# Optimization experiments

Measured on AMD Instinct MI355X. Metric: run time of the kernel, lower is better.

Reference implementation:

```python
import jax, jax.numpy as jnp
import numpy as np

ALPHA = 0.2  # leaky-relu negative slope


def setup_inputs() -> dict:
    key = jax.random.key(0)
    k1, k2, k3, k4 = jax.random.split(key, 4)
    bs, L, D, Fin, Fout = 4, 20000, 16, 128, 128
    x = jax.random.normal(k1, (bs, L, Fin), dtype=jnp.float32)
    adj = jax.random.randint(k2, (bs, L, D), 0, L, dtype=jnp.int64)
    # xavier_normal-ish init for W [Fin, Fout] and a [2*Fout, 1]
    W = jax.random.normal(k3, (Fin, Fout), dtype=jnp.float32) * (1.414 * np.sqrt(2.0 / (Fin + Fout))).astype(np.float32)
    a = jax.random.normal(k4, (2 * Fout, 1), dtype=jnp.float32) * (1.414 * np.sqrt(2.0 / (2 * Fout + 1))).astype(np.float32)
    return {"x": x, "adj": adj, "W": W, "a": a}


def reference(x, adj, W, a):
    Fout = W.shape[1]
    # gather fixed-degree neighbor features: [bs, L, D, Fin]
    nbr = jax.vmap(lambda xb, ab: xb[ab])(x, adj)
    h = jnp.matmul(nbr, W)  # [bs, L, D, Fout]
    # a is applied to cat([h_neighbor, h_center]); split it instead of concatenating
    a1 = a[:Fout, 0]
    a2 = a[Fout:, 0]
    # h[:, :, 0, :] is the center node (first neighbor slot, repeat_interleave in torch)
    e = jnp.einsum('bldf,f->bld', h, a1) + jnp.einsum('blf,f->bl', h[:, :, 0, :], a2)[..., None]
    attn = jax.nn.softmax(jax.nn.leaky_relu(e, ALPHA), axis=-1)  # softmax over D
    out = jnp.einsum('bld,bldf->blf', attn, h)  # weighted aggregate [bs, L, Fout]
    return jax.nn.elu(out)  # concat=True branch
```

## Files before the change

### kernel.cpp

```cpp
#include <hip/hip_runtime.h>
#include <hip/hip_bf16.h>

#define LSEQ 20000
#define DEG  16
#define F    128
#define ALPHA 0.2f

typedef __bf16 bf16x8 __attribute__((ext_vector_type(8)));
typedef float  f32x4  __attribute__((ext_vector_type(4)));

__device__ __forceinline__ float bf_lo(unsigned int u) { return __uint_as_float(u << 16); }
__device__ __forceinline__ float bf_hi(unsigned int u) { return __uint_as_float(u & 0xffff0000u); }
__device__ __forceinline__ float elu_f(float v) { return v > 0.f ? v : __expf(v) - 1.f; }

__global__ __launch_bounds__(256) void gat_wt(const float* __restrict__ W,
                                              const float* __restrict__ a,
                                              __hip_bfloat16* __restrict__ wt,
                                              float* __restrict__ wa)
{
    const int t = blockIdx.x * 256 + threadIdx.x;
    for (int i = t; i < F * F; i += 16 * 256) {
        const int k = i >> 7, n = i & (F - 1);
        wt[n * F + k] = __float2bfloat16(W[i]);
    }
    if (blockIdx.x == 0 && threadIdx.x < F) {
        const int k = threadIdx.x;
        float acc1 = 0.f, acc2 = 0.f;
        for (int n = 0; n < F; ++n) {
            const float w = W[k * F + n];
            acc1 = fmaf(w, a[n],     acc1);
            acc2 = fmaf(w, a[F + n], acc2);
        }
        wa[k]     = acc1;
        wa[F + k] = acc2;
    }
}

__global__ __launch_bounds__(256, 5) void gat_gemm(const float* __restrict__ x,
                                                   const __hip_bfloat16* __restrict__ wt,
                                                   const float* __restrict__ wa,
                                                   __hip_bfloat16* __restrict__ y16,
                                                   float* __restrict__ s1,
                                                   float* __restrict__ s2)
{
    __shared__ __hip_bfloat16 wl[F][F];

    const int t    = threadIdx.x;
    const int lane = t & 63;
    const int wid  = t >> 6;
    const int i0   = (blockIdx.x * 4 + wid) * 16;
    const int m    = lane & 15;
    const int q    = lane >> 4;

    {
        const uint4* wg = reinterpret_cast<const uint4*>(wt);
        #pragma unroll
        for (int i = 0; i < 8; ++i) {
            const int g   = t + 256 * i;
            const int row = g >> 4;
            const int c8  = g & 15;
            *reinterpret_cast<uint4*>(&wl[row][((c8 ^ (row & 7)) * 8)]) = wg[g];
        }
    }

    const float* xr = x + (size_t)(i0 + m) * F + q * 8;
    float4 xf[8];
    #pragma unroll
    for (int kt = 0; kt < 4; ++kt) {
        xf[2*kt]   = *reinterpret_cast<const float4*>(xr + kt * 32);
        xf[2*kt+1] = *reinterpret_cast<const float4*>(xr + kt * 32 + 4);
    }

    float p1 = 0.f, p2 = 0.f;
    {
        const float* w1p = wa + q * 8;
        const float* w2p = wa + F + q * 8;
        #pragma unroll
        for (int kt = 0; kt < 4; ++kt) {
            const float4 u0 = *reinterpret_cast<const float4*>(w1p + kt * 32);
            const float4 u1 = *reinterpret_cast<const float4*>(w1p + kt * 32 + 4);
            const float4 v0 = *reinterpret_cast<const float4*>(w2p + kt * 32);
            const float4 v1 = *reinterpret_cast<const float4*>(w2p + kt * 32 + 4);
            const float4 xa = xf[2*kt], xb = xf[2*kt+1];
            p1 = fmaf(xa.x,u0.x,p1); p1 = fmaf(xa.y,u0.y,p1);
            p1 = fmaf(xa.z,u0.z,p1); p1 = fmaf(xa.w,u0.w,p1);
            p1 = fmaf(xb.x,u1.x,p1); p1 = fmaf(xb.y,u1.y,p1);
            p1 = fmaf(xb.z,u1.z,p1); p1 = fmaf(xb.w,u1.w,p1);
            p2 = fmaf(xa.x,v0.x,p2); p2 = fmaf(xa.y,v0.y,p2);
            p2 = fmaf(xa.z,v0.z,p2); p2 = fmaf(xa.w,v0.w,p2);
            p2 = fmaf(xb.x,v1.x,p2); p2 = fmaf(xb.y,v1.y,p2);
            p2 = fmaf(xb.z,v1.z,p2); p2 = fmaf(xb.w,v1.w,p2);
        }
    }
    p1 += __shfl_xor(p1, 16); p1 += __shfl_xor(p1, 32);
    p2 += __shfl_xor(p2, 16); p2 += __shfl_xor(p2, 32);
    if (lane < 16) {
        s1[i0 + m] = p1;
        s2[i0 + m] = p2;
    }

    bf16x8 bfr[4];
    #pragma unroll
    for (int kt = 0; kt < 4; ++kt) {
        const float4 qa = xf[2*kt], qb = xf[2*kt+1];
        bf16x8 f;
        f[0] = (__bf16)qa.x; f[1] = (__bf16)qa.y; f[2] = (__bf16)qa.z; f[3] = (__bf16)qa.w;
        f[4] = (__bf16)qb.x; f[5] = (__bf16)qb.y; f[6] = (__bf16)qb.z; f[7] = (__bf16)qb.w;
        bfr[kt] = f;
    }

    __syncthreads();

    #pragma unroll
    for (int ct = 0; ct < 8; ++ct) {
        union { uint4 u; bf16x8 v; } afr[4];
        const int row = ct * 16 + m;
        #pragma unroll
        for (int kt = 0; kt < 4; ++kt)
            afr[kt].u = *reinterpret_cast<const uint4*>(
                            &wl[row][(((kt * 4 + q) ^ (m & 7)) * 8)]);

        f32x4 acc = {0.f, 0.f, 0.f, 0.f};
        #pragma unroll
        for (int kt = 0; kt < 4; ++kt)
            acc = __builtin_amdgcn_mfma_f32_16x16x32_bf16(afr[kt].v, bfr[kt], acc, 0, 0, 0);

        union { uint2 u; __hip_bfloat162 h[2]; } pk;
        pk.h[0] = __float22bfloat162_rn(make_float2(acc[0], acc[1]));
        pk.h[1] = __float22bfloat162_rn(make_float2(acc[2], acc[3]));
        *reinterpret_cast<uint2*>(y16 + (size_t)(i0 + m) * F + ct * 16 + q * 4) = pk.u;
    }
}

__global__ __launch_bounds__(256, 4) void gat_attn(const int* __restrict__ adj,
                                                   const __hip_bfloat16* __restrict__ y16,
                                                   const float* __restrict__ s1,
                                                   const float* __restrict__ s2,
                                                   float* __restrict__ out)
{
    const int lane  = threadIdx.x & 63;
    const int wid   = threadIdx.x >> 6;
    const int x8    = blockIdx.x & 7;
    const int j     = blockIdx.x >> 3;
    const int batch = x8 >> 1;
    const int grp   = j * 2 + (x8 & 1);
    const int base  = batch * LSEQ;
    const int g0    = base + grp * 16 + wid * 4;
    const int d     = lane & 15;
    const int g16   = lane & 48;

    const int av = adj[(size_t)g0 * DEG + lane];

    const float sv = s1[base + av];
    float s2l = (d == 0) ? s2[base + av] : 0.f;
    const float s2v = __shfl(s2l, g16);
    const float e = sv + s2v;
    const float t = e > 0.f ? e : ALPHA * e;

    float mx = t;
    #pragma unroll
    for (int off = 1; off < 16; off <<= 1) mx = fmaxf(mx, __shfl_xor(mx, off));
    const float w = __expf(t - mx);
    float p = w;
    #pragma unroll
    for (int off = 1; off < 16; off <<= 1) p += __shfl_xor(p, off);
    const float attn = w / p;

    const char* yb = reinterpret_cast<const char*>(y16 + ((size_t)base << 7)) + d * 16;
    float acc[8] = {0.f, 0.f, 0.f, 0.f, 0.f, 0.f, 0.f, 0.f};

    uint4 va[8], vb[8];
    #pragma unroll
    for (int k = 0; k < 8; ++k) {
        const int r = __shfl(av, g16 + k);
        va[k] = *reinterpret_cast<const uint4*>(yb + ((size_t)r << 8));
    }
    #pragma unroll
    for (int k = 0; k < 8; ++k) {
        const int r = __shfl(av, g16 + 8 + k);
        vb[k] = *reinterpret_cast<const uint4*>(yb + ((size_t)r << 8));
    }

    #pragma unroll
    for (int k = 0; k < 8; ++k) {
        const float wk = __shfl(attn, g16 + k);
        const uint4 v = va[k];
        acc[0] = fmaf(wk, bf_lo(v.x), acc[0]);
        acc[1] = fmaf(wk, bf_hi(v.x), acc[1]);
        acc[2] = fmaf(wk, bf_lo(v.y), acc[2]);
        acc[3] = fmaf(wk, bf_hi(v.y), acc[3]);
        acc[4] = fmaf(wk, bf_lo(v.z), acc[4]);
        acc[5] = fmaf(wk, bf_hi(v.z), acc[5]);
        acc[6] = fmaf(wk, bf_lo(v.w), acc[6]);
        acc[7] = fmaf(wk, bf_hi(v.w), acc[7]);
    }
    #pragma unroll
    for (int k = 0; k < 8; ++k) {
        const float wk = __shfl(attn, g16 + 8 + k);
        const uint4 v = vb[k];
        acc[0] = fmaf(wk, bf_lo(v.x), acc[0]);
        acc[1] = fmaf(wk, bf_hi(v.x), acc[1]);
        acc[2] = fmaf(wk, bf_lo(v.y), acc[2]);
        acc[3] = fmaf(wk, bf_hi(v.y), acc[3]);
        acc[4] = fmaf(wk, bf_lo(v.z), acc[4]);
        acc[5] = fmaf(wk, bf_hi(v.z), acc[5]);
        acc[6] = fmaf(wk, bf_lo(v.w), acc[6]);
        acc[7] = fmaf(wk, bf_hi(v.w), acc[7]);
    }

    float* op = out + (size_t)(g0 + (lane >> 4)) * F + d * 8;
    const float4 o0 = make_float4(elu_f(acc[0]), elu_f(acc[1]),
                                  elu_f(acc[2]), elu_f(acc[3]));
    const float4 o1 = make_float4(elu_f(acc[4]), elu_f(acc[5]),
                                  elu_f(acc[6]), elu_f(acc[7]));
    *reinterpret_cast<float4*>(op)     = o0;
    *reinterpret_cast<float4*>(op + 4) = o1;
}

extern "C" void kernel_launch(void* const* d_in, const int* in_sizes, int n_in,
                              void* d_out, int out_size, void* d_ws, size_t ws_size,
                              hipStream_t stream) {
    const float* x   = (const float*)d_in[0];
    const int*   adj = (const int*)d_in[1];
    const float* W   = (const float*)d_in[2];
    const float* a   = (const float*)d_in[3];
    float* out = (float*)d_out;

    const int BL = in_sizes[0] / F;

    __hip_bfloat16* y16 = (__hip_bfloat16*)d_ws;
    float* s1 = (float*)((char*)d_ws + (size_t)BL * F * sizeof(__hip_bfloat16));
    float* s2 = s1 + BL;
    __hip_bfloat16* wt = (__hip_bfloat16*)(s2 + BL);
    float* wa = (float*)(wt + F * F);

    gat_wt  <<<16, 256, 0, stream>>>(W, a, wt, wa);
    gat_gemm<<<BL / 64, 256, 0, stream>>>(x, wt, wa, y16, s1, s2);
    gat_attn<<<BL / 16, 256, 0, stream>>>(adj, y16, s1, s2, out);
}
```

Baseline: 137.6 us.

## Fuse GEMM and attention kernels into persistent kernel with grid barrier

```diff
diff --git a/kernel.cpp b/kernel.cpp
--- a/kernel.cpp
+++ b/kernel.cpp
@@ -5,6 +5,7 @@
 #define DEG  16
 #define F    128
 #define ALPHA 0.2f
+#define GRID 1024
 
 typedef __bf16 bf16x8 __attribute__((ext_vector_type(8)));
 typedef float  f32x4  __attribute__((ext_vector_type(4)));
@@ -13,10 +14,11 @@
 __device__ __forceinline__ float bf_hi(unsigned int u) { return __uint_as_float(u & 0xffff0000u); }
 __device__ __forceinline__ float elu_f(float v) { return v > 0.f ? v : __expf(v) - 1.f; }
 
-__global__ __launch_bounds__(256) void gat_wt(const float* __restrict__ W,
-                                              const float* __restrict__ a,
-                                              __hip_bfloat16* __restrict__ wt,
-                                              float* __restrict__ wa)
+__global__ __launch_bounds__(256) void gat_prep(const float* __restrict__ W,
+                                                const float* __restrict__ a,
+                                                __hip_bfloat16* __restrict__ wt,
+                                                float* __restrict__ wa,
+                                                unsigned int* __restrict__ bar)
 {
     const int t = blockIdx.x * 256 + threadIdx.x;
     for (int i = t; i < F * F; i += 16 * 256) {
@@ -34,23 +36,27 @@
         wa[k]     = acc1;
         wa[F + k] = acc2;
     }
+    if (blockIdx.x == 15 && threadIdx.x == 0) *bar = 0u;
 }
 
-__global__ __launch_bounds__(256, 5) void gat_gemm(const float* __restrict__ x,
-                                                   const __hip_bfloat16* __restrict__ wt,
-                                                   const float* __restrict__ wa,
-                                                   __hip_bfloat16* __restrict__ y16,
-                                                   float* __restrict__ s1,
-                                                   float* __restrict__ s2)
+__global__ __launch_bounds__(256, 4) void gat_fused(
+    const float* __restrict__ x,
+    const int*   __restrict__ adj,
+    const __hip_bfloat16* __restrict__ wt,
+    const float* __restrict__ wa,
+    __hip_bfloat16* __restrict__ y16,
+    float* __restrict__ s1,
+    float* __restrict__ s2,
+    float* __restrict__ out,
+    unsigned int* __restrict__ bar,
+    int BL)
 {
     __shared__ __hip_bfloat16 wl[F][F];
 
+    const int bid  = blockIdx.x;
     const int t    = threadIdx.x;
     const int lane = t & 63;
     const int wid  = t >> 6;
-    const int i0   = (blockIdx.x * 4 + wid) * 16;
-    const int m    = lane & 15;
-    const int q    = lane >> 4;
 
     {
         const uint4* wg = reinterpret_cast<const uint4*>(wt);
@@ -62,159 +68,173 @@
             *reinterpret_cast<uint4*>(&wl[row][((c8 ^ (row & 7)) * 8)]) = wg[g];
         }
     }
-
-    const float* xr = x + (size_t)(i0 + m) * F + q * 8;
-    float4 xf[8];
-    #pragma unroll
-    for (int kt = 0; kt < 4; ++kt) {
-        xf[2*kt]   = *reinterpret_cast<const float4*>(xr + kt * 32);
-        xf[2*kt+1] = *reinterpret_cast<const float4*>(xr + kt * 32 + 4);
-    }
-
-    float p1 = 0.f, p2 = 0.f;
+    __syncthreads();
+
+    const int m = lane & 15;
+    const int q = lane >> 4;
+    const int NU = BL / 64;
+
+    for (int u = bid; u < NU; u += GRID) {
+        const int i0 = u * 64 + wid * 16;
+
+        const float* xr = x + (size_t)(i0 + m) * F + q * 8;
+        float4 xf[8];
+        #pragma unroll
+        for (int kt = 0; kt < 4; ++kt) {
+            xf[2*kt]   = *reinterpret_cast<const float4*>(xr + kt * 32);
+            xf[2*kt+1] = *reinterpret_cast<const float4*>(xr + kt * 32 + 4);
+        }
+
+        float p1 = 0.f, p2 = 0.f;
+        {
+            const float* w1p = wa + q * 8;
+            const float* w2p = wa + F + q * 8;
+            #pragma unroll
+            for (int kt = 0; kt < 4; ++kt) {
+                const float4 u0 = *reinterpret_cast<const float4*>(w1p + kt * 32);
+                const float4 u1 = *reinterpret_cast<const float4*>(w1p + kt * 32 + 4);
+                const float4 v0 = *reinterpret_cast<const float4*>(w2p + kt * 32);
+                const float4 v1 = *reinterpret_cast<const float4*>(w2p + kt * 32 + 4);
+                const float4 xa = xf[2*kt], xb = xf[2*kt+1];
+                p1 = fmaf(xa.x,u0.x,p1); p1 = fmaf(xa.y,u0.y,p1);
+                p1 = fmaf(xa.z,u0.z,p1); p1 = fmaf(xa.w,u0.w,p1);
+                p1 = fmaf(xb.x,u1.x,p1); p1 = fmaf(xb.y,u1.y,p1);
+                p1 = fmaf(xb.z,u1.z,p1); p1 = fmaf(xb.w,u1.w,p1);
+                p2 = fmaf(xa.x,v0.x,p2); p2 = fmaf(xa.y,v0.y,p2);
+                p2 = fmaf(xa.z,v0.z,p2); p2 = fmaf(xa.w,v0.w,p2);
+                p2 = fmaf(xb.x,v1.x,p2); p2 = fmaf(xb.y,v1.y,p2);
+                p2 = fmaf(xb.z,v1.z,p2); p2 = fmaf(xb.w,v1.w,p2);
+            }
+        }
+        p1 += __shfl_xor(p1, 16); p1 += __shfl_xor(p1, 32);
+        p2 += __shfl_xor(p2, 16); p2 += __shfl_xor(p2, 32);
+        if (lane < 16) {
+            s1[i0 + m] = p1;
+            s2[i0 + m] = p2;
+        }
+
+        bf16x8 bfr[4];
+        #pragma unroll
+        for (int kt = 0; kt < 4; ++kt) {
+            const float4 qa = xf[2*kt], qb = xf[2*kt+1];
+            bf16x8 f;
+            f[0] = (__bf16)qa.x; f[1] = (__bf16)qa.y; f[2] = (__bf16)qa.z; f[3] = (__bf16)qa.w;
+            f[4] = (__bf16)qb.x; f[5] = (__bf16)qb.y; f[6] = (__bf16)qb.z; f[7] = (__bf16)qb.w;
+            bfr[kt] = f;
+        }
+
+        #pragma unroll
+        for (int ct = 0; ct < 8; ++ct) {
+            union { uint4 u; bf16x8 v; } afr[4];
+            const int row = ct * 16 + m;
+            #pragma unroll
+            for (int kt = 0; kt < 4; ++kt)
+                afr[kt].u = *reinterpret_cast<const uint4*>(
+                                &wl[row][(((kt * 4 + q) ^ (m & 7)) * 8)]);
+
+            f32x4 acc = {0.f, 0.f, 0.f, 0.f};
+            #pragma unroll
+            for (int kt = 0; kt < 4; ++kt)
+                acc = __builtin_amdgcn_mfma_f32_16x16x32_bf16(afr[kt].v, bfr[kt], acc, 0, 0, 0);
+
+            union { uint2 u; __hip_bfloat162 h[2]; } pk;
+            pk.h[0] = __float22bfloat162_rn(make_float2(acc[0], acc[1]));
+            pk.h[1] = __float22bfloat162_rn(make_float2(acc[2], acc[3]));
+            *reinterpret_cast<uint2*>(y16 + (size_t)(i0 + m) * F + ct * 16 + q * 4) = pk.u;
+        }
+    }
+
+    __syncthreads();
+    if (t == 0) {
+        __threadfence();
+        atomicAdd(bar, 1u);
+        while (atomicAdd(bar, 0u) < (unsigned)GRID)
+            __builtin_amdgcn_s_sleep(2);
+        __threadfence();
+    }
+    __syncthreads();
+
     {
-        const float* w1p = wa + q * 8;
-        const float* w2p = wa + F + q * 8;
-        #pragma unroll
-        for (int kt = 0; kt < 4; ++kt) {
-            const float4 u0 = *reinterpret_cast<const float4*>(w1p + kt * 32);
-            const float4 u1 = *reinterpret_cast<const float4*>(w1p + kt * 32 + 4);
-            const float4 v0 = *reinterpret_cast<const float4*>(w2p + kt * 32);
-            const float4 v1 = *reinterpret_cast<const float4*>(w2p + kt * 32 + 4);
-            const float4 xa = xf[2*kt], xb = xf[2*kt+1];
-            p1 = fmaf(xa.x,u0.x,p1); p1 = fmaf(xa.y,u0.y,p1);
-            p1 = fmaf(xa.z,u0.z,p1); p1 = fmaf(xa.w,u0.w,p1);
-            p1 = fmaf(xb.x,u1.x,p1); p1 = fmaf(xb.y,u1.y,p1);
-            p1 = fmaf(xb.z,u1.z,p1); p1 = fmaf(xb.w,u1.w,p1);
-            p2 = fmaf(xa.x,v0.x,p2); p2 = fmaf(xa.y,v0.y,p2);
-            p2 = fmaf(xa.z,v0.z,p2); p2 = fmaf(xa.w,v0.w,p2);
-            p2 = fmaf(xb.x,v1.x,p2); p2 = fmaf(xb.y,v1.y,p2);
-            p2 = fmaf(xb.z,v1.z,p2); p2 = fmaf(xb.w,v1.w,p2);
-        }
-    }
-    p1 += __shfl_xor(p1, 16); p1 += __shfl_xor(p1, 32);
-    p2 += __shfl_xor(p2, 16); p2 += __shfl_xor(p2, 32);
-    if (lane < 16) {
-        s1[i0 + m] = p1;
-        s2[i0 + m] = p2;
-    }
-
-    bf16x8 bfr[4];
-    #pragma unroll
-    for (int kt = 0; kt < 4; ++kt) {
-        const float4 qa = xf[2*kt], qb = xf[2*kt+1];
-        bf16x8 f;
-        f[0] = (__bf16)qa.x; f[1] = (__bf16)qa.y; f[2] = (__bf16)qa.z; f[3] = (__bf16)qa.w;
-        f[4] = (__bf16)qb.x; f[5] = (__bf16)qb.y; f[6] = (__bf16)qb.z; f[7] = (__bf16)qb.w;
-        bfr[kt] = f;
-    }
-
-    __syncthreads();
-
-    #pragma unroll
-    for (int ct = 0; ct < 8; ++ct) {
-        union { uint4 u; bf16x8 v; } afr[4];
-        const int row = ct * 16 + m;
-        #pragma unroll
-        for (int kt = 0; kt < 4; ++kt)
-            afr[kt].u = *reinterpret_cast<const uint4*>(
-                            &wl[row][(((kt * 4 + q) ^ (m & 7)) * 8)]);
-
-        f32x4 acc = {0.f, 0.f, 0.f, 0.f};
-        #pragma unroll
-        for (int kt = 0; kt < 4; ++kt)
-            acc = __builtin_amdgcn_mfma_f32_16x16x32_bf16(afr[kt].v, bfr[kt], acc, 0, 0, 0);
-
-        union { uint2 u; __hip_bfloat162 h[2]; } pk;
-        pk.h[0] = __float22bfloat162_rn(make_float2(acc[0], acc[1]));
-        pk.h[1] = __float22bfloat162_rn(make_float2(acc[2], acc[3]));
-        *reinterpret_cast<uint2*>(y16 + (size_t)(i0 + m) * F + ct * 16 + q * 4) = pk.u;
-    }
-}
-
-__global__ __launch_bounds__(256, 4) void gat_attn(const int* __restrict__ adj,
-                                                   const __hip_bfloat16* __restrict__ y16,
-                                                   const float* __restrict__ s1,
-                                                   const float* __restrict__ s2,
-                                                   float* __restrict__ out)
-{
-    const int lane  = threadIdx.x & 63;
-    const int wid   = threadIdx.x >> 6;
-    const int x8    = blockIdx.x & 7;
-    const int j     = blockIdx.x >> 3;
-    const int batch = x8 >> 1;
-    const int grp   = j * 2 + (x8 & 1);
-    const int base  = batch * LSEQ;
-    const int g0    = base + grp * 16 + wid * 4;
-    const int d     = lane & 15;
-    const int g16   = lane & 48;
-
-    const int av = adj[(size_t)g0 * DEG + lane];
-
-    const float sv = s1[base + av];
-    float s2l = (d == 0) ? s2[base + av] : 0.f;
-    const float s2v = __shfl(s2l, g16);
-    const float e = sv + s2v;
-    const float t = e > 0.f ? e : ALPHA * e;
-
-    float mx = t;
-    #pragma unroll
-    for (int off = 1; off < 16; off <<= 1) mx = fmaxf(mx, __shfl_xor(mx, off));
-    const float w = __expf(t - mx);
-    float p = w;
-    #pragma unroll
-    for (int off = 1; off < 16; off <<= 1) p += __shfl_xor(p, off);
-    const float attn = w / p;
-
-    const char* yb = reinterpret_cast<const char*>(y16 + ((size_t)base << 7)) + d * 16;
-    float acc[8] = {0.f, 0.f, 0.f, 0.f, 0.f, 0.f, 0.f, 0.f};
-
-    uint4 va[8], vb[8];
-    #pragma unroll
-    for (int k = 0; k < 8; ++k) {
-        const int r = __shfl(av, g16 + k);
-        va[k] = *reinterpret_cast<const uint4*>(yb + ((size_t)r << 8));
-    }
-    #pragma unroll
-    for (int k = 0; k < 8; ++k) {
-        const int r = __shfl(av, g16 + 8 + k);
-        vb[k] = *reinterpret_cast<const uint4*>(yb + ((size_t)r << 8));
-    }
-
-    #pragma unroll
-    for (int k = 0; k < 8; ++k) {
-        const float wk = __shfl(attn, g16 + k);
-        const uint4 v = va[k];
-        acc[0] = fmaf(wk, bf_lo(v.x), acc[0]);
-        acc[1] = fmaf(wk, bf_hi(v.x), acc[1]);
-        acc[2] = fmaf(wk, bf_lo(v.y), acc[2]);
-        acc[3] = fmaf(wk, bf_hi(v.y), acc[3]);
-        acc[4] = fmaf(wk, bf_lo(v.z), acc[4]);
-        acc[5] = fmaf(wk, bf_hi(v.z), acc[5]);
-        acc[6] = fmaf(wk, bf_lo(v.w), acc[6]);
-        acc[7] = fmaf(wk, bf_hi(v.w), acc[7]);
-    }
-    #pragma unroll
-    for (int k = 0; k < 8; ++k) {
-        const float wk = __shfl(attn, g16 + 8 + k);
-        const uint4 v = vb[k];
-        acc[0] = fmaf(wk, bf_lo(v.x), acc[0]);
-        acc[1] = fmaf(wk, bf_hi(v.x), acc[1]);
-        acc[2] = fmaf(wk, bf_lo(v.y), acc[2]);
-        acc[3] = fmaf(wk, bf_hi(v.y), acc[3]);
-        acc[4] = fmaf(wk, bf_lo(v.z), acc[4]);
-        acc[5] = fmaf(wk, bf_hi(v.z), acc[5]);
-        acc[6] = fmaf(wk, bf_lo(v.w), acc[6]);
-        acc[7] = fmaf(wk, bf_hi(v.w), acc[7]);
-    }
-
-    float* op = out + (size_t)(g0 + (lane >> 4)) * F + d * 8;
-    const float4 o0 = make_float4(elu_f(acc[0]), elu_f(acc[1]),
-                                  elu_f(acc[2]), elu_f(acc[3]));
-    const float4 o1 = make_float4(elu_f(acc[4]), elu_f(acc[5]),
-                                  elu_f(acc[6]), elu_f(acc[7]));
-    *reinterpret_cast<float4*>(op)     = o0;
-    *reinterpret_cast<float4*>(op + 4) = o1;
+        const int d   = lane & 15;
+        const int g16 = lane & 48;
+        const int NV  = BL / 16;
+
+        for (int v = bid; v < NV; v += GRID) {
+            const int x8    = v & 7;
+            const int j     = v >> 3;
+            const int batch = x8 >> 1;
+            const int grp   = j * 2 + (x8 & 1);
+            const int base  = batch * LSEQ;
+            const int g0    = base + grp * 16 + wid * 4;
+
+            const int av = adj[(size_t)g0 * DEG + lane];
+
+            const float sv = s1[base + av];
+            float s2l = (d == 0) ? s2[base + av] : 0.f;
+            const float s2v = __shfl(s2l, g16);
+            const float e = sv + s2v;
+            const float tv = e > 0.f ? e : ALPHA * e;
+
+            float mx = tv;
+            #pragma unroll
+            for (int off = 1; off < 16; off <<= 1) mx = fmaxf(mx, __shfl_xor(mx, off));
+            const float w = __expf(tv - mx);
+            float p = w;
+            #pragma unroll
+            for (int off = 1; off < 16; off <<= 1) p += __shfl_xor(p, off);
+            const float attn = w / p;
+
+            const char* yb = reinterpret_cast<const char*>(y16 + ((size_t)base << 7)) + d * 16;
+            float acc[8] = {0.f, 0.f, 0.f, 0.f, 0.f, 0.f, 0.f, 0.f};
+
+            uint4 va[8], vb[8];
+            #pragma unroll
+            for (int k = 0; k < 8; ++k) {
+                const int r = __shfl(av, g16 + k);
+                va[k] = *reinterpret_cast<const uint4*>(yb + ((size_t)r << 8));
+            }
+            #pragma unroll
+            for (int k = 0; k < 8; ++k) {
+                const int r = __shfl(av, g16 + 8 + k);
+                vb[k] = *reinterpret_cast<const uint4*>(yb + ((size_t)r << 8));
+            }
+
+            #pragma unroll
+            for (int k = 0; k < 8; ++k) {
+                const float wk = __shfl(attn, g16 + k);
+                const uint4 vv = va[k];
+                acc[0] = fmaf(wk, bf_lo(vv.x), acc[0]);
+                acc[1] = fmaf(wk, bf_hi(vv.x), acc[1]);
+                acc[2] = fmaf(wk, bf_lo(vv.y), acc[2]);
+                acc[3] = fmaf(wk, bf_hi(vv.y), acc[3]);
+                acc[4] = fmaf(wk, bf_lo(vv.z), acc[4]);
+                acc[5] = fmaf(wk, bf_hi(vv.z), acc[5]);
+                acc[6] = fmaf(wk, bf_lo(vv.w), acc[6]);
+                acc[7] = fmaf(wk, bf_hi(vv.w), acc[7]);
+            }
+            #pragma unroll
+            for (int k = 0; k < 8; ++k) {
+                const float wk = __shfl(attn, g16 + 8 + k);
+                const uint4 vv = vb[k];
+                acc[0] = fmaf(wk, bf_lo(vv.x), acc[0]);
+                acc[1] = fmaf(wk, bf_hi(vv.x), acc[1]);
+                acc[2] = fmaf(wk, bf_lo(vv.y), acc[2]);
+                acc[3] = fmaf(wk, bf_hi(vv.y), acc[3]);
+                acc[4] = fmaf(wk, bf_lo(vv.z), acc[4]);
+                acc[5] = fmaf(wk, bf_hi(vv.z), acc[5]);
+                acc[6] = fmaf(wk, bf_lo(vv.w), acc[6]);
+                acc[7] = fmaf(wk, bf_hi(vv.w), acc[7]);
+            }
+
+            float* op = out + (size_t)(g0 + (lane >> 4)) * F + d * 8;
+            const float4 o0 = make_float4(elu_f(acc[0]), elu_f(acc[1]),
+                                          elu_f(acc[2]), elu_f(acc[3]));
+            const float4 o1 = make_float4(elu_f(acc[4]), elu_f(acc[5]),
+                                          elu_f(acc[6]), elu_f(acc[7]));
+            *reinterpret_cast<float4*>(op)     = o0;
+            *reinterpret_cast<float4*>(op + 4) = o1;
+        }
+    }
 }
 
 extern "C" void kernel_launch(void* const* d_in, const int* in_sizes, int n_in,
@@ -233,8 +253,8 @@
     float* s2 = s1 + BL;
     __hip_bfloat16* wt = (__hip_bfloat16*)(s2 + BL);
     float* wa = (float*)(wt + F * F);
-
-    gat_wt  <<<16, 256, 0, stream>>>(W, a, wt, wa);
-    gat_gemm<<<BL / 64, 256, 0, stream>>>(x, wt, wa, y16, s1, s2);
-    gat_attn<<<BL / 16, 256, 0, stream>>>(adj, y16, s1, s2, out);
+    unsigned int* bar = (unsigned int*)(wa + 2 * F);
+
+    gat_prep <<<16,   256, 0, stream>>>(W, a, wt, wa, bar);
+    gat_fused<<<GRID, 256, 0, stream>>>(x, adj, wt, wa, y16, s1, s2, out, bar, BL);
 }
```

Measured after the change: 349.1 us. 154% more time.
